# Kernel optimization log

Hardware: AMD Instinct MI355X
Metric: run time of the kernel (lower is better)

Reference implementation:

```python
import jax, jax.numpy as jnp
import numpy as np

NS = [65536, 16384, 4096, 1024, 256, 64]          # nodes per level (64 = 8 graphs x 8 dense voxels)
ES = [1048576, 262144, 65536, 16384, 4096]        # edges per level (avg degree 16)
INS = [1, 15, 23, 31, 39]
OUTS = [12, 20, 28, 36, 44]
K = 5                                             # kernel_size


def setup_inputs():
    keys = iter(jax.random.split(jax.random.key(0), 64))
    d = {'x': jax.random.normal(next(keys), (NS[0], 1), jnp.float32),
         'pos': jax.random.uniform(next(keys), (NS[0], 3), jnp.float32)}
    for l in range(5):
        n, e, ci, co = NS[l], ES[l], INS[l], OUTS[l]
        d[f'src{l}'] = jax.random.randint(next(keys), (e,), 0, n)
        d[f'dst{l}'] = jax.random.randint(next(keys), (e,), 0, n)
        d[f'eattr{l}'] = jax.random.normal(next(keys), (e, 3), jnp.float32)
        d[f'cluster{l}'] = jax.random.randint(next(keys), (n,), 0, NS[l + 1])
        d[f'w1_{l}'] = jax.random.normal(next(keys), (3, K), jnp.float32) * 0.5
        d[f'b1_{l}'] = jnp.zeros((K,), jnp.float32)
        d[f'w2_{l}'] = jax.random.normal(next(keys), (K, ci * co), jnp.float32) / np.float32(np.sqrt(K * ci))
        d[f'b2_{l}'] = jnp.zeros((ci * co,), jnp.float32)
        d[f'root_{l}'] = jax.random.normal(next(keys), (ci, co), jnp.float32) / np.float32(np.sqrt(ci))
        d[f'bias_{l}'] = jnp.zeros((co,), jnp.float32)
    d['fc_w'] = jax.random.normal(next(keys), (8 * 47, 10), jnp.float32) / np.float32(np.sqrt(8 * 47))
    d['fc_b'] = jnp.zeros((10,), jnp.float32)
    return d


def _conv(x, src, dst, eattr, w1, b1, w2, b2, root, bias, n):
    # edge-conditioned kernel: MLP(edge_attr) -> [E, ci, co]
    h = jnp.tanh(eattr @ w1 + b1)                                  # [E, K]
    We = (h @ w2 + b2).reshape(eattr.shape[0], x.shape[1], -1)     # [E, ci, co]
    msg = jnp.einsum('ei,eio->eo', x[src], We)                     # gather + per-edge matvec
    s = jax.ops.segment_sum(msg, dst, num_segments=n)
    cnt = jax.ops.segment_sum(jnp.ones((dst.shape[0], 1), x.dtype), dst, num_segments=n)
    agg = s / jnp.maximum(cnt, 1.0)                                # mean aggregation
    return agg + x @ root + bias, jnp.mean(jnp.square(We))


def _pool(x, pos, cluster, n_next):
    # sparse voxel max pool on features, mean on positions; pos concatenated to features
    xm = jax.ops.segment_max(x, cluster, num_segments=n_next)
    xm = jnp.where(jnp.isfinite(xm), xm, 0.0)                      # empty voxels -> 0
    ps = jax.ops.segment_sum(pos, cluster, num_segments=n_next)
    cnt = jax.ops.segment_sum(jnp.ones((pos.shape[0], 1), pos.dtype), cluster, num_segments=n_next)
    pm = ps / jnp.maximum(cnt, 1.0)
    return jnp.concatenate([xm, pm], axis=1), pm


def reference(x, pos, src0, dst0, eattr0, cluster0, w1_0, b1_0, w2_0, b2_0, root_0, bias_0,
              src1, dst1, eattr1, cluster1, w1_1, b1_1, w2_1, b2_1, root_1, bias_1,
              src2, dst2, eattr2, cluster2, w1_2, b1_2, w2_2, b2_2, root_2, bias_2,
              src3, dst3, eattr3, cluster3, w1_3, b1_3, w2_3, b2_3, root_3, bias_3,
              src4, dst4, eattr4, cluster4, w1_4, b1_4, w2_4, b2_4, root_4, bias_4,
              fc_w, fc_b):
    lv = [(src0, dst0, eattr0, cluster0, w1_0, b1_0, w2_0, b2_0, root_0, bias_0),
          (src1, dst1, eattr1, cluster1, w1_1, b1_1, w2_1, b2_1, root_1, bias_1),
          (src2, dst2, eattr2, cluster2, w1_2, b1_2, w2_2, b2_2, root_2, bias_2),
          (src3, dst3, eattr3, cluster3, w1_3, b1_3, w2_3, b2_3, root_3, bias_3),
          (src4, dst4, eattr4, cluster4, w1_4, b1_4, w2_4, b2_4, root_4, bias_4)]
    closs = jnp.float32(0.0)
    for l, (src, dst, ea, cl, w1, b1, w2, b2, rt, bs) in enumerate(lv):
        x, c = _conv(x, src, dst, ea, w1, b1, w2, b2, rt, bs, NS[l])
        closs = closs + c
        x, pos = _pool(x, pos, cl, NS[l + 1])
    feat = x.reshape(-1, 8 * 47)                                   # [B, 8*47]
    logits = feat @ fc_w + fc_b
    return jax.nn.log_softmax(logits, axis=1), closs
```

## Files before the change

### kernel.cpp

```cpp
#include <hip/hip_runtime.h>
#include <hip/hip_fp16.h>
#include <math.h>


#define TILES0 1024
#define TSZ0   1024
#define NB0    512
#define TILES1 256
#define TSZ1   1024
#define NB1    512

__device__ __forceinline__ float ftanh(float x) {
    float e = __expf(2.f * x);
    return 1.f - 2.f / (e + 1.f);
}

struct SegArgs {
    const int* idx[10];
    int*       cnt[10];
    int*       rp [10];
    int*       out[10];
    int        n  [10];
    int        nb [10];
    int        tstart[11];
};

struct ScanAux {
    int* tilesum;
    int* tileoff;
    int  sstart[11];
    int  T;
};

struct HArgs {
    const float* eattr[5];
    const float* w1[5];
    const float* b1[5];
    float*       H;
    int          E[5];
    int          bstart[6];
};

struct WArgs {
    const float* w2[5];
    const float* b2[5];
    const float* H;
    float*       sq;
    int          cico[5];
    int          E[5];
};

__global__ __launch_bounds__(256) void countA_k(
    SegArgs a, HArgs ha, const int* __restrict__ dst0,
    const int* __restrict__ dst1, int* __restrict__ M, int* __restrict__ M1,
    int hsBlocks)
{
    __shared__ int sh[NB0];
    int B = blockIdx.x;
    int t = threadIdx.x;

    if (B < TILES0) {
        for (int u = t; u < NB0; u += 256) sh[u] = 0;
        __syncthreads();
        int base = B * TSZ0 + t;
        #pragma unroll
        for (int it = 0; it < 4; it++)
            atomicAdd(&sh[dst0[base + it * 256] >> 7], 1);
        __syncthreads();
        for (int u = t; u < NB0; u += 256) M[(size_t)B * NB0 + u] = sh[u];
        return;
    }
    B -= TILES0;
    if (B < TILES1) {
        for (int u = t; u < NB1; u += 256) sh[u] = 0;
        __syncthreads();
        int base = B * TSZ1 + t;
        #pragma unroll
        for (int it = 0; it < 4; it++)
            atomicAdd(&sh[dst1[base + it * 256] >> 5], 1);
        __syncthreads();
        for (int u = t; u < NB1; u += 256) M1[(size_t)B * NB1 + u] = sh[u];
        return;
    }
    B -= TILES1;
    if (B < hsBlocks) {
        const int K = 8;
        int l = 0;
        while (l < 4 && B >= ha.bstart[l + 1]) l++;
        int bloc = B - ha.bstart[l];
        const float* ea = ha.eattr[l];
        float w1r[15], b1r[5];
        #pragma unroll
        for (int i = 0; i < 15; i++) w1r[i] = ha.w1[l][i];
        #pragma unroll
        for (int i = 0; i < 5; i++)  b1r[i] = ha.b1[l][i];
        float acc[20];
        #pragma unroll
        for (int i = 0; i < 20; i++) acc[i] = 0.f;
        int base = bloc * 256 * K + t;
        for (int it = 0; it < K; it++) {
            int e = base + it * 256;
            if (e < ha.E[l]) {
                float e0 = ea[e * 3], e1 = ea[e * 3 + 1], e2 = ea[e * 3 + 2];
                float h[5];
                #pragma unroll
                for (int k = 0; k < 5; k++)
                    h[k] = ftanh(e0 * w1r[k] + e1 * w1r[5 + k] + e2 * w1r[10 + k] + b1r[k]);
                int p = 5;
                #pragma unroll
                for (int k = 0; k < 5; k++) {
                    acc[k] += h[k];
                    #pragma unroll
                    for (int k2 = k; k2 < 5; k2++) acc[p++] += h[k] * h[k2];
                }
            }
        }
        float* red = (float*)sh;
        int wid = t >> 6, lane = t & 63;
        #pragma unroll
        for (int v = 0; v < 20; v++) {
            float s = acc[v];
            #pragma unroll
            for (int o = 32; o; o >>= 1) s += __shfl_down(s, o);
            if (lane == 0) red[wid * 20 + v] = s;
        }
        __syncthreads();
        if (t < 20)
            atomicAdd(&ha.H[l * 20 + t],
                      red[t] + red[20 + t] + red[40 + t] + red[60 + t]);
        return;
    }
    B -= hsBlocks;
    {
        int s = 0;
        while (s < 9 && B >= a.tstart[s + 1]) s++;
        int i0 = (B - a.tstart[s]) * 1024;
        const int* idx = a.idx[s];
        int* cnt = a.cnt[s];
        int n = a.n[s];
        #pragma unroll
        for (int j = 0; j < 4; j++) {
            int i = i0 + j * 256 + t;
            if (i < n) atomicAdd(&cnt[idx[i]], 1);
        }
    }
}

__global__ __launch_bounds__(256) void scanP1_k(
    SegArgs a, ScanAux x, const int* __restrict__ M, int* __restrict__ M2,
    int* __restrict__ colTotal, const int* __restrict__ M1,
    int* __restrict__ M21, int* __restrict__ ct1)
{
    __shared__ int sc[256];
    int B = blockIdx.x;
    int t = threadIdx.x;

    if (B < NB0) {
        int v[4];
        int s4 = 0;
        #pragma unroll
        for (int j = 0; j < 4; j++) {
            v[j] = M[(size_t)(t * 4 + j) * NB0 + B];
            s4 += v[j];
        }
        sc[t] = s4;
        __syncthreads();
        for (int d = 1; d < 256; d <<= 1) {
            int u = (t >= d) ? sc[t - d] : 0;
            __syncthreads();
            sc[t] += u;
            __syncthreads();
        }
        int run = sc[t] - s4;
        #pragma unroll
        for (int j = 0; j < 4; j++) {
            M2[(size_t)(t * 4 + j) * NB0 + B] = run;
            run += v[j];
        }
        if (t == 255) colTotal[B] = sc[255];
        return;
    }
    B -= NB0;
    if (B < NB1) {
        int v = M1[(size_t)t * NB1 + B];
        sc[t] = v;
        __syncthreads();
        for (int d = 1; d < 256; d <<= 1) {
            int u = (t >= d) ? sc[t - d] : 0;
            __syncthreads();
            sc[t] += u;
            __syncthreads();
        }
        M21[(size_t)t * NB1 + B] = sc[t] - v;
        if (t == 255) ct1[B] = sc[255];
        return;
    }
    int b = B - NB1;
    int s = 0;
    while (s < 9 && b >= x.sstart[s + 1]) s++;
    int tloc = b - x.sstart[s];
    int nb = a.nb[s];
    const int* cnt = a.cnt[s];
    int i0 = tloc * 4096 + t * 16;
    int sum = 0;
    #pragma unroll
    for (int k = 0; k < 16; k++) {
        int i = i0 + k;
        if (i < nb) sum += cnt[i];
    }
    #pragma unroll
    for (int o = 32; o; o >>= 1) sum += __shfl_down(sum, o);
    if ((t & 63) == 0) sc[t >> 6] = sum;
    __syncthreads();
    if (t == 0)
        x.tilesum[b] = sc[0] + sc[1] + sc[2] + sc[3];
}

__global__ __launch_bounds__(512) void scanP2_k(
    SegArgs a, ScanAux x, const int* __restrict__ colTotal,
    int* __restrict__ bucketStart, const int* __restrict__ ct1,
    int* __restrict__ bs1)
{
    __shared__ int sc[NB0];
    int t = threadIdx.x;
    if (blockIdx.x == 0) {
        int v = colTotal[t];
        sc[t] = v;
        __syncthreads();
        for (int d = 1; d < NB0; d <<= 1) {
            int u = (t >= d) ? sc[t - d] : 0;
            __syncthreads();
            sc[t] += u;
            __syncthreads();
        }
        bucketStart[t] = sc[t] - v;
        if (t == NB0 - 1) bucketStart[NB0] = sc[NB0 - 1];
        return;
    }
    if (blockIdx.x == 2) {
        int v = ct1[t];
        sc[t] = v;
        __syncthreads();
        for (int d = 1; d < NB1; d <<= 1) {
            int u = (t >= d) ? sc[t - d] : 0;
            __syncthreads();
            sc[t] += u;
            __syncthreads();
        }
        bs1[t] = sc[t] - v;
        if (t == NB1 - 1) bs1[NB1] = sc[NB1 - 1];
        return;
    }
    if (t >= 64) return;
    int lane = t;
    int orig = (lane < x.T) ? x.tilesum[lane] : 0;
    int val = orig;
    #pragma unroll
    for (int d = 1; d < 64; d <<= 1) {
        int v = __shfl_up(val, d);
        if (lane >= d) val += v;
    }
    int excl = val - orig;
    int s = 0;
    while (s < 9 && lane >= x.sstart[s + 1]) s++;
    int segExcl = __shfl(excl, x.sstart[s]);
    if (lane < x.T) {
        x.tileoff[lane] = excl - segExcl;
        if (lane == x.sstart[s + 1] - 1)
            a.rp[s][a.nb[s]] = val - segExcl;
    }
}

__global__ __launch_bounds__(256) void scanP3_k(
    SegArgs a, ScanAux x,
    const int* __restrict__ src, const int* __restrict__ dst,
    const float* __restrict__ ea, const float* __restrict__ x0,
    const int* __restrict__ M2, const int* __restrict__ bucketStart,
    float4* __restrict__ pay2,
    const float* __restrict__ w1, const float* __restrict__ b1,
    float* __restrict__ H0,
    const int* __restrict__ src1, const int* __restrict__ dst1,
    const float* __restrict__ ea1, const int* __restrict__ M21,
    const int* __restrict__ bs1, float4* __restrict__ pay1)
{
    __shared__ int   shi[NB0];
    __shared__ float shf[100];
    int B = blockIdx.x;
    int t = threadIdx.x;

    if (B < TILES0) {
        int tile = B;
        for (int u = t; u < NB0; u += 256)
            shi[u] = bucketStart[u] + M2[(size_t)tile * NB0 + u];
        if (t < 15) shf[t] = w1[t];
        if (t >= 32 && t < 37) shf[15 + t - 32] = b1[t - 32];
        __syncthreads();

        float acc[20];
        #pragma unroll
        for (int i = 0; i < 20; i++) acc[i] = 0.f;

        int base = tile * TSZ0 + t;
        #pragma unroll
        for (int it = 0; it < 4; it++) {
            int i = base + it * 256;
            int d = dst[i];
            float e0 = ea[i * 3], e1 = ea[i * 3 + 1], e2 = ea[i * 3 + 2];
            float h[5];
            #pragma unroll
            for (int k = 0; k < 5; k++)
                h[k] = ftanh(e0 * shf[k] + e1 * shf[5 + k] + e2 * shf[10 + k] + shf[15 + k]);
            int p = 5;
            #pragma unroll
            for (int k = 0; k < 5; k++) {
                acc[k] += h[k];
                #pragma unroll
                for (int k2 = k; k2 < 5; k2++) acc[p++] += h[k] * h[k2];
            }
            float xv = x0[src[i]];
            union HU { __half2 h2; float f; } p01, p23;
            p01.h2 = __floats2half2_rn(h[0], h[1]);
            p23.h2 = __floats2half2_rn(h[2], h[3]);
            unsigned wbits = ((unsigned)d << 16) |
                             (unsigned)__half_as_ushort(__float2half_rn(h[4]));
            int ps = atomicAdd(&shi[d >> 7], 1);
            pay2[ps] = make_float4(xv, p01.f, p23.f, __uint_as_float(wbits));
        }

        int wid = t >> 6, lane = t & 63;
        #pragma unroll
        for (int v = 0; v < 20; v++) {
            float s = acc[v];
            #pragma unroll
            for (int o = 32; o; o >>= 1) s += __shfl_down(s, o);
            if (lane == 0) shf[20 + wid * 20 + v] = s;
        }
        __syncthreads();
        if (t < 20)
            atomicAdd(&H0[t], shf[20 + t] + shf[40 + t] + shf[60 + t] + shf[80 + t]);
        return;
    }
    B -= TILES0;
    if (B < TILES1) {
        int tile = B;
        for (int u = t; u < NB1; u += 256)
            shi[u] = bs1[u] + M21[(size_t)tile * NB1 + u];
        __syncthreads();
        int base = tile * TSZ1 + t;
        #pragma unroll
        for (int it = 0; it < 4; it++) {
            int i = base + it * 256;
            int d = dst1[i];
            int key = (d << 16) | src1[i];
            float e0 = ea1[i * 3], e1 = ea1[i * 3 + 1], e2 = ea1[i * 3 + 2];
            int ps = atomicAdd(&shi[d >> 5], 1);
            pay1[ps] = make_float4(__int_as_float(key), e0, e1, e2);
        }
        return;
    }
    B -= TILES1;
    int s = 0;
    while (s < 9 && B >= x.sstart[s + 1]) s++;
    int tloc = B - x.sstart[s];
    int nb = a.nb[s];
    const int* cnt = a.cnt[s];
    int* rp = a.rp[s];
    int i0 = tloc * 4096 + t * 16;
    int v[16];
    int sum = 0;
    #pragma unroll
    for (int k = 0; k < 16; k++) {
        int i = i0 + k;
        v[k] = (i < nb) ? cnt[i] : 0;
        sum += v[k];
    }
    int acc = sum;
    shi[t] = acc;
    __syncthreads();
    for (int d = 1; d < 256; d <<= 1) {
        int t2 = (t >= d) ? shi[t - d] : 0;
        __syncthreads();
        acc += t2;
        shi[t] = acc;
        __syncthreads();
    }
    int running = x.tileoff[B] + (acc - sum);
    #pragma unroll
    for (int k = 0; k < 16; k++) {
        int i = i0 + k;
        if (i < nb) rp[i] = running;
        running += v[k];
    }
}

__global__ __launch_bounds__(256) void scatC_k(
    SegArgs a, WArgs wa,
    const float4* __restrict__ pay2, const int* __restrict__ bucketStart,
    const float* __restrict__ w2, const float* __restrict__ b2,
    const float* __restrict__ root, const float* __restrict__ bias,
    const float* __restrict__ x, float* __restrict__ y,
    const float4* __restrict__ pay1, const int* __restrict__ bs1,
    int* __restrict__ rp1, float4* __restrict__ rec1)
{
    __shared__ float wsm[96];
    __shared__ float nacc[7 * 128];
    __shared__ int hist[32], st[32], cur[32];
    int B = blockIdx.x;
    int t = threadIdx.x;

    if (B < NB0) {
        if (t < 60) wsm[t] = w2[t];
        else if (t >= 64  && t < 76)  wsm[60 + t - 64]  = b2[t - 64];
        else if (t >= 128 && t < 140) wsm[72 + t - 128] = root[t - 128];
        else if (t >= 192 && t < 204) wsm[84 + t - 192] = bias[t - 192];
        for (int u = t; u < 7 * 128; u += 256) nacc[u] = 0.f;
        __syncthreads();

        int lo = bucketStart[B], hi = bucketStart[B + 1];
        int bin0 = B << 7;
        for (int j = lo + t; j < hi; j += 256) {
            float4 R = pay2[j];
            union HU { float f; __half2 h2; } a01, a23;
            a01.f = R.y; a23.f = R.z;
            unsigned wbits = __float_as_uint(R.w);
            int node = (int)(wbits >> 16) - bin0;
            float xv = R.x;
            atomicAdd(&nacc[node], xv);
            atomicAdd(&nacc[128 + node], __low2float(a01.h2)  * xv);
            atomicAdd(&nacc[256 + node], __high2float(a01.h2) * xv);
            atomicAdd(&nacc[384 + node], __low2float(a23.h2)  * xv);
            atomicAdd(&nacc[512 + node], __high2float(a23.h2) * xv);
            atomicAdd(&nacc[640 + node],
                      __half2float(__ushort_as_half((unsigned short)(wbits & 0xffffu))) * xv);
            atomicAdd(&nacc[768 + node], 1.f);
        }
        __syncthreads();

        if (t < 128) {
            int v = bin0 + t;
            float deg = nacc[768 + t];
            float S0 = nacc[t],       S1 = nacc[128 + t], S2 = nacc[256 + t];
            float S3 = nacc[384 + t], S4 = nacc[512 + t], S5 = nacc[640 + t];
            float inv = 1.f / fmaxf(deg, 1.f);
            float xv = x[v];
            #pragma unroll
            for (int o = 0; o < 12; o++) {
                float msg = wsm[60 + o] * S0 + wsm[o] * S1 + wsm[12 + o] * S2 +
                            wsm[24 + o] * S3 + wsm[36 + o] * S4 + wsm[48 + o] * S5;
                y[v * 12 + o] = msg * inv + xv * wsm[72 + o] + wsm[84 + o];
            }
        }
        return;
    }
    B -= NB0;
    if (B < NB1) {
        int b = B;
        int lo = bs1[b], hi = bs1[b + 1];
        int bin0 = b << 5;
        if (t < 32) hist[t] = 0;
        __syncthreads();
        const float* payw = (const float*)pay1;
        for (int j = lo + t; j < hi; j += 256) {
            int rel = (int)(__float_as_uint(payw[4 * j]) >> 16) - bin0;
            atomicAdd(&hist[rel], 1);
        }
        __syncthreads();
        if (t < 32) {
            int v = hist[t];
            int val = v;
            #pragma unroll
            for (int d = 1; d < 32; d <<= 1) {
                int u = __shfl_up(val, d);
                if (t >= d) val += u;
            }
            st[t] = val - v;
            cur[t] = lo + val - v;
            rp1[bin0 + t] = lo + val - v;
            if (b == NB1 - 1 && t == 31) rp1[NB1 * 32] = hi;
        }
        __syncthreads();
        for (int j = lo + t; j < hi; j += 256) {
            float4 R = pay1[j];
            int rel = (int)(__float_as_uint(R.x) >> 16) - bin0;
            int p = atomicAdd(&cur[rel], 1);
            rec1[p] = R;
        }
        return;
    }
    B -= NB1;
    if (B < 5) {
        if (t >= 64) return;
        int l = B;
        const float* w2l = wa.w2[l];
        const float* b2l = wa.b2[l];
        int cico = wa.cico[l];
        float d[21];
        #pragma unroll
        for (int i = 0; i < 21; i++) d[i] = 0.f;
        for (int u = t; u < cico; u += 64) {
            float b = b2l[u];
            float w[5];
            #pragma unroll
            for (int k = 0; k < 5; k++) w[k] = w2l[k * cico + u];
            int p = 0;
            #pragma unroll
            for (int k = 0; k < 5; k++) {
                #pragma unroll
                for (int k2 = k; k2 < 5; k2++) d[p++] += w[k] * w[k2];
            }
            #pragma unroll
            for (int k = 0; k < 5; k++) d[15 + k] += b * w[k];
            d[20] += b * b;
        }
        #pragma unroll
        for (int i = 0; i < 21; i++) {
            #pragma unroll
            for (int off = 32; off; off >>= 1) d[i] += __shfl_down(d[i], off);
        }
        if (t == 0) {
            const float* H1 = wa.H + l * 20;
            const float* H2 = H1 + 5;
            float sq = (float)wa.E[l] * d[20];
            #pragma unroll
            for (int k = 0; k < 5; k++) sq += 2.f * d[15 + k] * H1[k];
            int p = 0;
            #pragma unroll
            for (int k = 0; k < 5; k++) {
                #pragma unroll
                for (int k2 = k; k2 < 5; k2++) {
                    sq += ((k == k2) ? 1.f : 2.f) * d[p] * H2[p];
                    p++;
                }
            }
            wa.sq[l] = sq;
        }
        return;
    }
    B -= 5;
    {
        int s = 0;
        while (s < 9 && B >= a.tstart[s + 1]) s++;
        int i0 = (B - a.tstart[s]) * 1024;
        const int* idx = a.idx[s];
        int* cnt = a.cnt[s];
        const int* rp = a.rp[s];
        int* out = a.out[s];
        int n = a.n[s];
        #pragma unroll
        for (int j = 0; j < 4; j++) {
            int i = i0 + j * 256 + t;
            if (i < n) {
                int d = idx[i];
                int p = atomicSub(&cnt[d], 1) - 1;
                out[rp[d] + p] = i;
            }
        }
    }
}

__global__ __launch_bounds__(256) void conv1s_k(
    const int* __restrict__ rp, const float4* __restrict__ rec,
    const float* __restrict__ w1, const float* __restrict__ b1,
    const float* __restrict__ w2, const float* __restrict__ b2,
    const float* __restrict__ root, const float* __restrict__ bias,
    const float* __restrict__ x, float* __restrict__ y)
{
    constexpr int CI = 15, CO = 20, CH = 48, CICO = CI * CO;
    __shared__ float w1s[20];
    __shared__ float4 recb[CH];
    __shared__ int   svb[CH];
    __shared__ float hb[CH * 6];
    __shared__ float xs[CH * CI];
    __shared__ float S[6 * CI];

    int t = threadIdx.x;
    int v = blockIdx.x;
    if (t < 20) w1s[t] = (t < 15) ? w1[t] : b1[t - 15];
    int r0 = rp[v], r1 = rp[v + 1];
    int d  = r1 - r0;
    float acc = 0.f;

    for (int c0 = r0; c0 < r1; c0 += CH) {
        int cn = min(CH, r1 - c0);
        if (t < cn) {
            float4 R = rec[c0 + t];
            recb[t] = R;
            svb[t]  = (int)(__float_as_uint(R.x) & 0xffffu);
            hb[t * 6] = 1.f;
        }
        __syncthreads();
        if (t < cn * 5) {
            int j = t / 5, k = t % 5;
            float e0 = recb[j].y, e1 = recb[j].z, e2 = recb[j].w;
            hb[j * 6 + 1 + k] =
                ftanh(e0 * w1s[k] + e1 * w1s[5 + k] + e2 * w1s[10 + k] + w1s[15 + k]);
        }
        for (int u = t; u < cn * CI; u += 256)
            xs[u] = x[(size_t)svb[u / CI] * CI + (u % CI)];
        __syncthreads();
        if (t < 6 * CI) {
            int i = t / 6, k6 = t % 6;
            for (int j = 0; j < cn; j++)
                acc += hb[j * 6 + k6] * xs[j * CI + i];
        }
        __syncthreads();
    }

    if (t < 6 * CI) S[t] = acc;
    __syncthreads();

    if (t < CO) {
        float m = 0.f;
        for (int i = 0; i < CI; i++) {
            m += b2[i * CO + t] * S[i * 6];
            #pragma unroll
            for (int k = 0; k < 5; k++)
                m += w2[k * CICO + i * CO + t] * S[i * 6 + 1 + k];
        }
        m /= fmaxf((float)d, 1.f);
        for (int i = 0; i < CI; i++)
            m += x[(size_t)v * CI + i] * root[i * CO + t];
        y[(size_t)v * CO + t] = m + bias[t];
    }
}

template<int CI, int CO>
__global__ __launch_bounds__(256) void coop_conv_k(
    const int* __restrict__ rp, const int* __restrict__ eid,
    const int* __restrict__ src, const float* __restrict__ eattr,
    const float* __restrict__ w1, const float* __restrict__ b1,
    const float* __restrict__ w2, const float* __restrict__ b2,
    const float* __restrict__ root, const float* __restrict__ bias,
    const float* __restrict__ x, float* __restrict__ y)
{
    constexpr int CH   = 48;
    constexpr int CICO = CI * CO;
    __shared__ float w1s[20];
    __shared__ int   eb[CH], svb[CH];
    __shared__ float hb[CH * 6];
    __shared__ float xs[CH * CI];
    __shared__ float S[6 * CI];

    int t = threadIdx.x;
    int v = blockIdx.x;
    if (t < 20) w1s[t] = (t < 15) ? w1[t] : b1[t - 15];
    int r0 = rp[v], r1 = rp[v + 1];
    int d  = r1 - r0;
    float acc = 0.f;

    for (int c0 = r0; c0 < r1; c0 += CH) {
        int cn = min(CH, r1 - c0);
        if (t < cn) {
            int e = eid[c0 + t];
            eb[t]  = e;
            svb[t] = src[e];
            hb[t * 6] = 1.f;
        }
        __syncthreads();
        if (t < cn * 5) {
            int j = t / 5, k = t % 5;
            int e = eb[j];
            float e0 = eattr[e * 3], e1 = eattr[e * 3 + 1], e2 = eattr[e * 3 + 2];
            hb[j * 6 + 1 + k] =
                ftanh(e0 * w1s[k] + e1 * w1s[5 + k] + e2 * w1s[10 + k] + w1s[15 + k]);
        }
        for (int u = t; u < cn * CI; u += 256)
            xs[u] = x[(size_t)svb[u / CI] * CI + (u % CI)];
        __syncthreads();
        if (t < 6 * CI) {
            int i = t / 6, k6 = t % 6;
            for (int j = 0; j < cn; j++)
                acc += hb[j * 6 + k6] * xs[j * CI + i];
        }
        __syncthreads();
    }

    if (t < 6 * CI) S[t] = acc;
    __syncthreads();

    if (t < CO) {
        float m = 0.f;
        for (int i = 0; i < CI; i++) {
            m += b2[i * CO + t] * S[i * 6];
            #pragma unroll
            for (int k = 0; k < 5; k++)
                m += w2[k * CICO + i * CO + t] * S[i * 6 + 1 + k];
        }
        m /= fmaxf((float)d, 1.f);
        for (int i = 0; i < CI; i++)
            m += x[(size_t)v * CI + i] * root[i * CO + t];
        y[(size_t)v * CO + t] = m + bias[t];
    }
}

template<int CO>
__global__ __launch_bounds__(256) void pool_k(
    int NN,
    const int* __restrict__ crp, const int* __restrict__ cnid,
    const float* __restrict__ y, const float* __restrict__ pos,
    float* __restrict__ xn, float* __restrict__ pn)
{
    int t = blockIdx.x * 256 + threadIdx.x;
    if (t >= NN * (CO + 3)) return;
    int c = t / (CO + 3), o = t % (CO + 3);
    int r0 = crp[c], r1 = crp[c + 1];
    int d = r1 - r0;
    if (o < CO) {
        float m = -INFINITY;
        for (int j = r0; j < r1; j++)
            m = fmaxf(m, y[(size_t)cnid[j] * CO + o]);
        if (d == 0 || !isfinite(m)) m = 0.f;
        xn[c * (CO + 3) + o] = m;
    } else {
        int k = o - CO;
        float sum = 0.f;
        for (int j = r0; j < r1; j++)
            sum += pos[cnid[j] * 3 + k];
        float pm = sum / fmaxf((float)d, 1.f);
        xn[c * (CO + 3) + CO + k] = pm;
        pn[c * 3 + k] = pm;
    }
}

__global__ __launch_bounds__(128) void fc_k(
    const float* __restrict__ x5,
    const float* __restrict__ fc_w, const float* __restrict__ fc_b,
    const float* __restrict__ sq, float* __restrict__ out)
{
    __shared__ float feat[8 * 376];
    __shared__ float logit[80];
    __shared__ float roff[8];
    for (int t = threadIdx.x; t < 8 * 376; t += 128) feat[t] = x5[t];
    __syncthreads();
    int t = threadIdx.x;
    if (t < 80) {
        int b = t / 10, j = t % 10;
        float acc = fc_b[j];
        for (int k = 0; k < 376; k++) acc += feat[b * 376 + k] * fc_w[k * 10 + j];
        logit[t] = acc;
    }
    __syncthreads();
    if (t < 8) {
        float m = -1e30f;
        for (int j = 0; j < 10; j++) m = fmaxf(m, logit[t * 10 + j]);
        float ssum = 0.f;
        for (int j = 0; j < 10; j++) ssum += expf(logit[t * 10 + j] - m);
        roff[t] = m + logf(ssum);
    }
    __syncthreads();
    if (t < 80) out[t] = logit[t] - roff[t / 10];
    if (t == 0) {
        float closs = 0.f;
        closs += sq[0] * (1.0f / 12582912.0f);
        closs += sq[1] * (1.0f / 78643200.0f);
        closs += sq[2] * (1.0f / 42205184.0f);
        closs += sq[3] * (1.0f / 18284544.0f);
        closs += sq[4] * (1.0f / 7028736.0f);
        out[80] = closs;
    }
}


extern "C" void kernel_launch(void* const* d_in, const int* in_sizes, int n_in,
                              void* d_out, int out_size, void* d_ws, size_t ws_size,
                              hipStream_t stream)
{
    static const int NSa[6] = {65536, 16384, 4096, 1024, 256, 64};
    static const int ESa[5] = {1048576, 262144, 65536, 16384, 4096};
    static const int COa[5] = {12, 20, 28, 36, 44};
    static const int CIa[5] = {1, 15, 23, 31, 39};

    const float* x0   = (const float*)d_in[0];
    const float* pos0 = (const float*)d_in[1];

    int* wsw = (int*)d_ws;
    size_t off = 0;
    auto alw = [&](size_t n) -> size_t {
        size_t p = off; off += (n + 63) & ~(size_t)63; return p;
    };
    size_t degO[5], cdegO[5];
    for (int l = 2; l < 5; l++) degO[l]  = alw(NSa[l]);
    for (int l = 0; l < 5; l++) cdegO[l] = alw(NSa[l + 1]);
    size_t HO = alw(100);
    size_t zeroWords = off;
    size_t rpO[5], crpO[5], eidO[5], cnidO[5];
    rpO[1] = alw(NSa[1] + 1);
    for (int l = 2; l < 5; l++) rpO[l]  = alw(NSa[l] + 1);
    for (int l = 0; l < 5; l++) crpO[l] = alw(NSa[l + 1] + 1);
    for (int l = 2; l < 5; l++) eidO[l] = alw(ESa[l]);
    for (int l = 0; l < 5; l++) cnidO[l] = alw(NSa[l]);
    size_t tsO  = alw(64);
    size_t toO  = alw(64);
    size_t MO   = alw((size_t)TILES0 * NB0);
    size_t M2O  = alw((size_t)TILES0 * NB0);
    size_t ctO  = alw(NB0);
    size_t bsO  = alw(NB0 + 1);
    size_t payO = alw((size_t)ESa[0] * 4);
    size_t M1O  = alw((size_t)TILES1 * NB1);
    size_t M21O = alw((size_t)TILES1 * NB1);
    size_t ct1O = alw(NB1);
    size_t bs1O = alw(NB1 + 1);
    size_t pay1O = alw((size_t)ESa[1] * 4);
    size_t rec1O = alw((size_t)ESa[1] * 4);
    size_t yO   = alw((size_t)65536 * 12);
    size_t sqO  = alw(8);
    size_t xnO[5], pnO[5];
    for (int l = 0; l < 5; l++) xnO[l] = alw((size_t)NSa[l + 1] * (COa[l] + 3));
    for (int l = 0; l < 5; l++) pnO[l] = alw((size_t)NSa[l] * 3 / 4 + 64);
    for (int l = 0; l < 5; l++) pnO[l] = alw((size_t)NSa[l + 1] * 3);

    hipMemsetAsync(d_ws, 0, zeroWords * 4, stream);

    SegArgs sa{};
    int nseg = 0;
    for (int l = 2; l < 5; l++) {
        sa.idx[nseg] = (const int*)d_in[3 + 10 * l];
        sa.cnt[nseg] = wsw + degO[l];
        sa.rp [nseg] = wsw + rpO[l];
        sa.out[nseg] = wsw + eidO[l];
        sa.n  [nseg] = ESa[l];
        sa.nb [nseg] = NSa[l];
        nseg++;
    }
    for (int l = 0; l < 5; l++) {
        sa.idx[nseg] = (const int*)d_in[5 + 10 * l];
        sa.cnt[nseg] = wsw + cdegO[l];
        sa.rp [nseg] = wsw + crpO[l];
        sa.out[nseg] = wsw + cnidO[l];
        sa.n  [nseg] = NSa[l];
        sa.nb [nseg] = NSa[l + 1];
        nseg++;
    }
    ScanAux sx{};
    int tiles = 0, btiles = 0;
    for (int s = 0; s < nseg; s++) {
        sa.tstart[s] = tiles;
        tiles += (sa.n[s] + 1023) / 1024;
        sx.sstart[s] = btiles;
        btiles += (sa.nb[s] + 4095) / 4096;
    }
    for (int s = nseg; s <= 10; s++) {
        sa.tstart[s] = tiles;
        sx.sstart[s] = btiles;
        if (s < 10) {
            sa.idx[s] = sa.idx[nseg - 1]; sa.cnt[s] = sa.cnt[nseg - 1];
            sa.rp[s] = sa.rp[nseg - 1];   sa.out[s] = sa.out[nseg - 1];
            sa.n[s] = 0; sa.nb[s] = 8;
        }
    }
    sx.T = btiles;
    sx.tilesum = wsw + tsO;
    sx.tileoff = wsw + toO;

    float4* pay2 = (float4*)(wsw + payO);
    float4* pay1 = (float4*)(wsw + pay1O);
    float4* rec1 = (float4*)(wsw + rec1O);
    float*  Hp   = (float*)(wsw + HO);

    HArgs ha{};
    int bs = 0;
    ha.bstart[0] = 0;
    ha.eattr[0] = (const float*)d_in[4];
    ha.w1[0] = (const float*)d_in[6];
    ha.b1[0] = (const float*)d_in[7];
    ha.E[0] = 0;
    for (int l = 1; l < 5; l++) {
        ha.eattr[l] = (const float*)d_in[4 + 10 * l];
        ha.w1[l]    = (const float*)d_in[6 + 10 * l];
        ha.b1[l]    = (const float*)d_in[7 + 10 * l];
        ha.E[l]     = ESa[l];
        ha.bstart[l] = bs;
        bs += (ESa[l] + 2047) / 2048;
    }
    ha.bstart[5] = bs;
    ha.H = Hp;

    WArgs wa{};
    for (int l = 0; l < 5; l++) {
        wa.w2[l]   = (const float*)d_in[8 + 10 * l];
        wa.b2[l]   = (const float*)d_in[9 + 10 * l];
        wa.cico[l] = CIa[l] * COa[l];
        wa.E[l]    = ESa[l];
    }
    wa.H  = Hp;
    wa.sq = (float*)(wsw + sqO);

    countA_k<<<TILES0 + TILES1 + bs + tiles, 256, 0, stream>>>(
        sa, ha, (const int*)d_in[3], (const int*)d_in[13],
        wsw + MO, wsw + M1O, bs);
    scanP1_k<<<NB0 + NB1 + btiles, 256, 0, stream>>>(
        sa, sx, wsw + MO, wsw + M2O, wsw + ctO,
        wsw + M1O, wsw + M21O, wsw + ct1O);
    scanP2_k<<<3, 512, 0, stream>>>(sa, sx, wsw + ctO, wsw + bsO,
                                    wsw + ct1O, wsw + bs1O);
    scanP3_k<<<TILES0 + TILES1 + btiles, 256, 0, stream>>>(
        sa, sx,
        (const int*)d_in[2], (const int*)d_in[3], (const float*)d_in[4],
        x0, wsw + M2O, wsw + bsO, pay2,
        (const float*)d_in[6], (const float*)d_in[7], Hp,
        (const int*)d_in[12], (const int*)d_in[13], (const float*)d_in[14],
        wsw + M21O, wsw + bs1O, pay1);

    float* yb = (float*)(wsw + yO);

    scatC_k<<<NB0 + NB1 + 5 + tiles, 256, 0, stream>>>(
        sa, wa, pay2, wsw + bsO,
        (const float*)d_in[8], (const float*)d_in[9],
        (const float*)d_in[10], (const float*)d_in[11], x0, yb,
        pay1, wsw + bs1O, wsw + rpO[1], rec1);

    pool_k<12><<<(NSa[1] * 15 + 255) / 256, 256, 0, stream>>>(
        NSa[1], wsw + crpO[0], wsw + cnidO[0], yb, pos0,
        (float*)(wsw + xnO[0]), (float*)(wsw + pnO[0]));

    conv1s_k<<<NSa[1], 256, 0, stream>>>(
        wsw + rpO[1], rec1,
        (const float*)d_in[16], (const float*)d_in[17],
        (const float*)d_in[18], (const float*)d_in[19],
        (const float*)d_in[20], (const float*)d_in[21],
        (const float*)(wsw + xnO[0]), yb);
    pool_k<20><<<(NSa[2] * 23 + 255) / 256, 256, 0, stream>>>(
        NSa[2], wsw + crpO[1], wsw + cnidO[1], yb,
        (const float*)(wsw + pnO[0]),
        (float*)(wsw + xnO[1]), (float*)(wsw + pnO[1]));

#define LVLC(l, CI_, CO_) do {                                                 \
    const float* xin   = (const float*)(wsw + xnO[(l) - 1]);                   \
    const float* posin = (const float*)(wsw + pnO[(l) - 1]);                   \
    int N = NSa[(l)], NN = NSa[(l) + 1];                                       \
    coop_conv_k<CI_, CO_><<<N, 256, 0, stream>>>(                              \
        wsw + rpO[(l)], wsw + eidO[(l)],                                       \
        (const int*)d_in[2 + 10 * (l)], (const float*)d_in[4 + 10 * (l)],      \
        (const float*)d_in[6 + 10 * (l)], (const float*)d_in[7 + 10 * (l)],    \
        (const float*)d_in[8 + 10 * (l)], (const float*)d_in[9 + 10 * (l)],    \
        (const float*)d_in[10 + 10 * (l)], (const float*)d_in[11 + 10 * (l)],  \
        xin, yb);                                                              \
    pool_k<CO_><<<(NN * ((CO_) + 3) + 255) / 256, 256, 0, stream>>>(           \
        NN, wsw + crpO[(l)], wsw + cnidO[(l)], yb, posin,                      \
        (float*)(wsw + xnO[(l)]), (float*)(wsw + pnO[(l)]));                   \
} while (0)

    LVLC(2, 23, 28);
    LVLC(3, 31, 36);
    LVLC(4, 39, 44);
#undef LVLC

    fc_k<<<1, 128, 0, stream>>>((const float*)(wsw + xnO[4]),
                                (const float*)d_in[52], (const float*)d_in[53],
                                wa.sq, (float*)d_out);
}
```

Measured before the change: 403.6 us.

## Replace level-0 edge sort with per-node moment atomics and fuse pooling into convs

Level-0 edges are no longer bucket-sorted into a payload. Because ci=1, each edge instead atomically adds x_src and h_k*x_src into a per-destination 8-float accumulator, and the node output is rebuilt algebraically from those sums with w2/b2. Max pooling is done with atomicMax on order-preserving encoded floats into raw per-cluster rows, so the separate pool kernels and cluster CSR scans go away. The launch chain drops from around 14 to 9 kernels. In exchange it adds heavy global float atomics (7 per edge over 1M edges) and makes the float summation order nondeterministic.

```diff
diff --git a/kernel.cpp b/kernel.cpp
--- a/kernel.cpp
+++ b/kernel.cpp
@@ -3,9 +3,6 @@
 #include <math.h>
 
 
-#define TILES0 1024
-#define TSZ0   1024
-#define NB0    512
 #define TILES1 256
 #define TSZ1   1024
 #define NB1    512
@@ -15,92 +12,143 @@
     return 1.f - 2.f / (e + 1.f);
 }
 
-struct SegArgs {
-    const int* idx[10];
-    int*       cnt[10];
-    int*       rp [10];
-    int*       out[10];
-    int        n  [10];
-    int        nb [10];
-    int        tstart[11];
+__device__ __forceinline__ unsigned fenc(float f) {
+    int b = __float_as_int(f);
+    return (b < 0) ? ~(unsigned)b : ((unsigned)b | 0x80000000u);
+}
+__device__ __forceinline__ float fdec(unsigned u) {
+    int b = (u & 0x80000000u) ? (int)(u & 0x7fffffffu) : ~(int)u;
+    return __int_as_float(b);
+}
+
+__device__ __forceinline__ float row_val(const unsigned* __restrict__ row,
+                                         int i, int CI) {
+    float cn = __uint_as_float(row[CI]);
+    if (i < CI - 3) return (cn == 0.f) ? 0.f : fdec(row[i]);
+    return __uint_as_float(row[i]) / fmaxf(cn, 1.f);
+}
+
+struct Seg3 {
+    const int* idx[3];
+    int*       cnt[3];
+    int*       rp [3];
+    int*       out[3];
+    int        n  [3];
+    int        nb [3];
+    int        tstart[4];
 };
 
-struct ScanAux {
-    int* tilesum;
-    int* tileoff;
-    int  sstart[11];
-    int  T;
+struct GA {
+    const int *src0, *dst0; const float* ea0;
+    const int *src1, *dst1; const float* ea1;
+    const float *x0, *pos0;
+    const int* cluster[5];
+    const float *w1[5], *b1[5], *w2[5], *b2[5], *root[5], *bias[5];
+    const int* srcE[3]; const float* eaE[3];
+    const float *fc_w, *fc_b;
+    float* S0;
+    unsigned* raw[5];
+    float* H; float* sq;
+    int *M1, *M21, *bktTot, *bs1;
+    float4 *pay1, *rec1; int* rp1;
+    Seg3 sg;
+    float* out;
+    const float* hea[4]; int hE[4]; int hb0[5];
+    int hsB, tiles;
 };
 
-struct HArgs {
-    const float* eattr[5];
-    const float* w1[5];
-    const float* b1[5];
-    float*       H;
-    int          E[5];
-    int          bstart[6];
-};
-
-struct WArgs {
-    const float* w2[5];
-    const float* b2[5];
-    const float* H;
-    float*       sq;
-    int          cico[5];
-    int          E[5];
-};
-
-__global__ __launch_bounds__(256) void countA_k(
-    SegArgs a, HArgs ha, const int* __restrict__ dst0,
-    const int* __restrict__ dst1, int* __restrict__ M, int* __restrict__ M1,
-    int hsBlocks)
+__global__ __launch_bounds__(256) void k1_fuseA(GA A)
 {
-    __shared__ int sh[NB0];
-    int B = blockIdx.x;
-    int t = threadIdx.x;
-
-    if (B < TILES0) {
-        for (int u = t; u < NB0; u += 256) sh[u] = 0;
-        __syncthreads();
-        int base = B * TSZ0 + t;
-        #pragma unroll
-        for (int it = 0; it < 4; it++)
-            atomicAdd(&sh[dst0[base + it * 256] >> 7], 1);
-        __syncthreads();
-        for (int u = t; u < NB0; u += 256) M[(size_t)B * NB0 + u] = sh[u];
+    __shared__ int sh[NB1];
+    int B = blockIdx.x, t = threadIdx.x;
+
+    if (B < 1024) {
+        float w1r[15], b1r[5];
+        #pragma unroll
+        for (int i = 0; i < 15; i++) w1r[i] = A.w1[0][i];
+        #pragma unroll
+        for (int i = 0; i < 5; i++)  b1r[i] = A.b1[0][i];
+        float acc[20];
+        #pragma unroll
+        for (int i = 0; i < 20; i++) acc[i] = 0.f;
+        int base = B * 1024 + t;
+        #pragma unroll
+        for (int it = 0; it < 4; it++) {
+            int i = base + it * 256;
+            int sv = A.src0[i], d = A.dst0[i];
+            float e0 = A.ea0[i * 3], e1 = A.ea0[i * 3 + 1], e2 = A.ea0[i * 3 + 2];
+            float h[5];
+            #pragma unroll
+            for (int k = 0; k < 5; k++)
+                h[k] = ftanh(e0 * w1r[k] + e1 * w1r[5 + k] + e2 * w1r[10 + k] + b1r[k]);
+            int p = 5;
+            #pragma unroll
+            for (int k = 0; k < 5; k++) {
+                acc[k] += h[k];
+                #pragma unroll
+                for (int k2 = k; k2 < 5; k2++) acc[p++] += h[k] * h[k2];
+            }
+            float xv = A.x0[sv];
+            float* Sr = A.S0 + (size_t)d * 8;
+            atomicAdd(&Sr[0], xv);
+            atomicAdd(&Sr[1], h[0] * xv);
+            atomicAdd(&Sr[2], h[1] * xv);
+            atomicAdd(&Sr[3], h[2] * xv);
+            atomicAdd(&Sr[4], h[3] * xv);
+            atomicAdd(&Sr[5], h[4] * xv);
+            atomicAdd(&Sr[6], 1.f);
+        }
+        float* red = (float*)sh;
+        int wid = t >> 6, lane = t & 63;
+        #pragma unroll
+        for (int v = 0; v < 20; v++) {
+            float s = acc[v];
+            #pragma unroll
+            for (int o = 32; o; o >>= 1) s += __shfl_down(s, o);
+            if (lane == 0) red[wid * 20 + v] = s;
+        }
+        __syncthreads();
+        if (t < 20)
+            atomicAdd(&A.H[t], red[t] + red[20 + t] + red[40 + t] + red[60 + t]);
         return;
     }
-    B -= TILES0;
+    B -= 1024;
     if (B < TILES1) {
         for (int u = t; u < NB1; u += 256) sh[u] = 0;
         __syncthreads();
         int base = B * TSZ1 + t;
         #pragma unroll
         for (int it = 0; it < 4; it++)
-            atomicAdd(&sh[dst1[base + it * 256] >> 5], 1);
-        __syncthreads();
-        for (int u = t; u < NB1; u += 256) M1[(size_t)B * NB1 + u] = sh[u];
+            atomicAdd(&sh[A.dst1[base + it * 256] >> 5], 1);
+        __syncthreads();
+        for (int u = t; u < NB1; u += 256) {
+            int c = sh[u];
+            A.M1[(size_t)B * NB1 + u] = c;
+            if (c) atomicAdd(&A.bktTot[u], c);
+        }
         return;
     }
     B -= TILES1;
-    if (B < hsBlocks) {
+    if (B < A.hsB) {
         const int K = 8;
-        int l = 0;
-        while (l < 4 && B >= ha.bstart[l + 1]) l++;
-        int bloc = B - ha.bstart[l];
-        const float* ea = ha.eattr[l];
+        int j = 0;
+        while (j < 3 && B >= A.hb0[j + 1]) j++;
+        int bloc = B - A.hb0[j];
+        const float* ea = A.hea[j];
+        const float* w1p = A.w1[j + 1];
+        const float* b1p = A.b1[j + 1];
         float w1r[15], b1r[5];
         #pragma unroll
-        for (int i = 0; i < 15; i++) w1r[i] = ha.w1[l][i];
-        #pragma unroll
-        for (int i = 0; i < 5; i++)  b1r[i] = ha.b1[l][i];
+        for (int i = 0; i < 15; i++) w1r[i] = w1p[i];
+        #pragma unroll
+        for (int i = 0; i < 5; i++)  b1r[i] = b1p[i];
         float acc[20];
         #pragma unroll
         for (int i = 0; i < 20; i++) acc[i] = 0.f;
         int base = bloc * 256 * K + t;
         for (int it = 0; it < K; it++) {
             int e = base + it * 256;
-            if (e < ha.E[l]) {
+            if (e < A.hE[j]) {
                 float e0 = ea[e * 3], e1 = ea[e * 3 + 1], e2 = ea[e * 3 + 2];
                 float h[5];
                 #pragma unroll
@@ -126,18 +174,18 @@
         }
         __syncthreads();
         if (t < 20)
-            atomicAdd(&ha.H[l * 20 + t],
+            atomicAdd(&A.H[(j + 1) * 20 + t],
                       red[t] + red[20 + t] + red[40 + t] + red[60 + t]);
         return;
     }
-    B -= hsBlocks;
+    B -= A.hsB;
     {
         int s = 0;
-        while (s < 9 && B >= a.tstart[s + 1]) s++;
-        int i0 = (B - a.tstart[s]) * 1024;
-        const int* idx = a.idx[s];
-        int* cnt = a.cnt[s];
-        int n = a.n[s];
+        while (s < 2 && B >= A.sg.tstart[s + 1]) s++;
+        int i0 = (B - A.sg.tstart[s]) * 1024;
+        const int* idx = A.sg.idx[s];
+        int* cnt = A.sg.cnt[s];
+        int n = A.sg.n[s];
         #pragma unroll
         for (int j = 0; j < 4; j++) {
             int i = i0 + j * 256 + t;
@@ -146,24 +194,43 @@
     }
 }
 
-__global__ __launch_bounds__(256) void scanP1_k(
-    SegArgs a, ScanAux x, const int* __restrict__ M, int* __restrict__ M2,
-    int* __restrict__ colTotal, const int* __restrict__ M1,
-    int* __restrict__ M21, int* __restrict__ ct1)
+__global__ __launch_bounds__(256) void k2_fuseB(GA A)
 {
     __shared__ int sc[256];
-    int B = blockIdx.x;
-    int t = threadIdx.x;
-
-    if (B < NB0) {
-        int v[4];
-        int s4 = 0;
-        #pragma unroll
-        for (int j = 0; j < 4; j++) {
-            v[j] = M[(size_t)(t * 4 + j) * NB0 + B];
-            s4 += v[j];
-        }
-        sc[t] = s4;
+    __shared__ float wsm[96];
+    int B = blockIdx.x, t = threadIdx.x;
+
+    if (B < 256) {
+        if (t < 60) wsm[t] = A.w2[0][t];
+        else if (t >= 64  && t < 76)  wsm[60 + t - 64]  = A.b2[0][t - 64];
+        else if (t >= 128 && t < 140) wsm[72 + t - 128] = A.root[0][t - 128];
+        else if (t >= 192 && t < 204) wsm[84 + t - 192] = A.bias[0][t - 192];
+        __syncthreads();
+        int v = B * 256 + t;
+        const float* Sr = A.S0 + (size_t)v * 8;
+        float s0 = Sr[0], s1 = Sr[1], s2 = Sr[2], s3 = Sr[3], s4 = Sr[4], s5 = Sr[5];
+        float dg = Sr[6];
+        float inv = 1.f / fmaxf(dg, 1.f);
+        float xv = A.x0[v];
+        int c = A.cluster[0][v];
+        unsigned* orow = A.raw[0] + (size_t)c * 16;
+        #pragma unroll
+        for (int o = 0; o < 12; o++) {
+            float m = (wsm[60 + o] * s0 + wsm[o] * s1 + wsm[12 + o] * s2 +
+                       wsm[24 + o] * s3 + wsm[36 + o] * s4 + wsm[48 + o] * s5) * inv +
+                      xv * wsm[72 + o] + wsm[84 + o];
+            atomicMax(&orow[o], fenc(m));
+        }
+        atomicAdd((float*)&orow[12], A.pos0[v * 3]);
+        atomicAdd((float*)&orow[13], A.pos0[v * 3 + 1]);
+        atomicAdd((float*)&orow[14], A.pos0[v * 3 + 2]);
+        atomicAdd((float*)&orow[15], 1.f);
+        return;
+    }
+    B -= 256;
+    if (B < NB1) {
+        int v = A.M1[(size_t)t * NB1 + B];
+        sc[t] = v;
         __syncthreads();
         for (int d = 1; d < 256; d <<= 1) {
             int u = (t >= d) ? sc[t - d] : 0;
@@ -171,19 +238,14 @@
             sc[t] += u;
             __syncthreads();
         }
-        int run = sc[t] - s4;
-        #pragma unroll
-        for (int j = 0; j < 4; j++) {
-            M2[(size_t)(t * 4 + j) * NB0 + B] = run;
-            run += v[j];
-        }
-        if (t == 255) colTotal[B] = sc[255];
+        A.M21[(size_t)t * NB1 + B] = sc[t] - v;
         return;
     }
-    B -= NB0;
-    if (B < NB1) {
-        int v = M1[(size_t)t * NB1 + B];
-        sc[t] = v;
+    B -= NB1;
+    if (B < 1) {
+        int a0 = A.bktTot[2 * t], a1 = A.bktTot[2 * t + 1];
+        int ps = a0 + a1;
+        sc[t] = ps;
         __syncthreads();
         for (int d = 1; d < 256; d <<= 1) {
             int u = (t >= d) ? sc[t - d] : 0;
@@ -191,309 +253,55 @@
             sc[t] += u;
             __syncthreads();
         }
-        M21[(size_t)t * NB1 + B] = sc[t] - v;
-        if (t == 255) ct1[B] = sc[255];
+        int excl = sc[t] - ps;
+        A.bs1[2 * t]     = excl;
+        A.bs1[2 * t + 1] = excl + a0;
+        if (t == 255) A.bs1[512] = sc[255];
         return;
     }
-    int b = B - NB1;
-    int s = 0;
-    while (s < 9 && b >= x.sstart[s + 1]) s++;
-    int tloc = b - x.sstart[s];
-    int nb = a.nb[s];
-    const int* cnt = a.cnt[s];
-    int i0 = tloc * 4096 + t * 16;
-    int sum = 0;
-    #pragma unroll
-    for (int k = 0; k < 16; k++) {
-        int i = i0 + k;
-        if (i < nb) sum += cnt[i];
-    }
-    #pragma unroll
-    for (int o = 32; o; o >>= 1) sum += __shfl_down(sum, o);
-    if ((t & 63) == 0) sc[t >> 6] = sum;
-    __syncthreads();
-    if (t == 0)
-        x.tilesum[b] = sc[0] + sc[1] + sc[2] + sc[3];
-}
-
-__global__ __launch_bounds__(512) void scanP2_k(
-    SegArgs a, ScanAux x, const int* __restrict__ colTotal,
-    int* __restrict__ bucketStart, const int* __restrict__ ct1,
-    int* __restrict__ bs1)
-{
-    __shared__ int sc[NB0];
-    int t = threadIdx.x;
-    if (blockIdx.x == 0) {
-        int v = colTotal[t];
-        sc[t] = v;
-        __syncthreads();
-        for (int d = 1; d < NB0; d <<= 1) {
-            int u = (t >= d) ? sc[t - d] : 0;
+    B -= 1;
+    if (B < 3) {
+        int s = B;
+        int nb = A.sg.nb[s];
+        const int* cnt = A.sg.cnt[s];
+        int* rp = A.sg.rp[s];
+        int i0 = t * 16;
+        int v[16];
+        int sum = 0;
+        #pragma unroll
+        for (int k = 0; k < 16; k++) {
+            int i = i0 + k;
+            v[k] = (i < nb) ? cnt[i] : 0;
+            sum += v[k];
+        }
+        int acc = sum;
+        sc[t] = acc;
+        __syncthreads();
+        for (int d = 1; d < 256; d <<= 1) {
+            int t2 = (t >= d) ? sc[t - d] : 0;
             __syncthreads();
-            sc[t] += u;
+            acc += t2;
+            sc[t] = acc;
             __syncthreads();
         }
-        bucketStart[t] = sc[t] - v;
-        if (t == NB0 - 1) bucketStart[NB0] = sc[NB0 - 1];
+        int running = acc - sum;
+        #pragma unroll
+        for (int k = 0; k < 16; k++) {
+            int i = i0 + k;
+            if (i < nb) rp[i] = running;
+            running += v[k];
+        }
+        if (i0 + 16 == nb) rp[nb] = running;
         return;
     }
-    if (blockIdx.x == 2) {
-        int v = ct1[t];
-        sc[t] = v;
-        __syncthreads();
-        for (int d = 1; d < NB1; d <<= 1) {
-            int u = (t >= d) ? sc[t - d] : 0;
-            __syncthreads();
-            sc[t] += u;
-            __syncthreads();
-        }
-        bs1[t] = sc[t] - v;
-        if (t == NB1 - 1) bs1[NB1] = sc[NB1 - 1];
-        return;
-    }
-    if (t >= 64) return;
-    int lane = t;
-    int orig = (lane < x.T) ? x.tilesum[lane] : 0;
-    int val = orig;
-    #pragma unroll
-    for (int d = 1; d < 64; d <<= 1) {
-        int v = __shfl_up(val, d);
-        if (lane >= d) val += v;
-    }
-    int excl = val - orig;
-    int s = 0;
-    while (s < 9 && lane >= x.sstart[s + 1]) s++;
-    int segExcl = __shfl(excl, x.sstart[s]);
-    if (lane < x.T) {
-        x.tileoff[lane] = excl - segExcl;
-        if (lane == x.sstart[s + 1] - 1)
-            a.rp[s][a.nb[s]] = val - segExcl;
-    }
-}
-
-__global__ __launch_bounds__(256) void scanP3_k(
-    SegArgs a, ScanAux x,
-    const int* __restrict__ src, const int* __restrict__ dst,
-    const float* __restrict__ ea, const float* __restrict__ x0,
-    const int* __restrict__ M2, const int* __restrict__ bucketStart,
-    float4* __restrict__ pay2,
-    const float* __restrict__ w1, const float* __restrict__ b1,
-    float* __restrict__ H0,
-    const int* __restrict__ src1, const int* __restrict__ dst1,
-    const float* __restrict__ ea1, const int* __restrict__ M21,
-    const int* __restrict__ bs1, float4* __restrict__ pay1)
-{
-    __shared__ int   shi[NB0];
-    __shared__ float shf[100];
-    int B = blockIdx.x;
-    int t = threadIdx.x;
-
-    if (B < TILES0) {
-        int tile = B;
-        for (int u = t; u < NB0; u += 256)
-            shi[u] = bucketStart[u] + M2[(size_t)tile * NB0 + u];
-        if (t < 15) shf[t] = w1[t];
-        if (t >= 32 && t < 37) shf[15 + t - 32] = b1[t - 32];
-        __syncthreads();
-
-        float acc[20];
-        #pragma unroll
-        for (int i = 0; i < 20; i++) acc[i] = 0.f;
-
-        int base = tile * TSZ0 + t;
-        #pragma unroll
-        for (int it = 0; it < 4; it++) {
-            int i = base + it * 256;
-            int d = dst[i];
-            float e0 = ea[i * 3], e1 = ea[i * 3 + 1], e2 = ea[i * 3 + 2];
-            float h[5];
-            #pragma unroll
-            for (int k = 0; k < 5; k++)
-                h[k] = ftanh(e0 * shf[k] + e1 * shf[5 + k] + e2 * shf[10 + k] + shf[15 + k]);
-            int p = 5;
-            #pragma unroll
-            for (int k = 0; k < 5; k++) {
-                acc[k] += h[k];
-                #pragma unroll
-                for (int k2 = k; k2 < 5; k2++) acc[p++] += h[k] * h[k2];
-            }
-            float xv = x0[src[i]];
-            union HU { __half2 h2; float f; } p01, p23;
-            p01.h2 = __floats2half2_rn(h[0], h[1]);
-            p23.h2 = __floats2half2_rn(h[2], h[3]);
-            unsigned wbits = ((unsigned)d << 16) |
-                             (unsigned)__half_as_ushort(__float2half_rn(h[4]));
-            int ps = atomicAdd(&shi[d >> 7], 1);
-            pay2[ps] = make_float4(xv, p01.f, p23.f, __uint_as_float(wbits));
-        }
-
-        int wid = t >> 6, lane = t & 63;
-        #pragma unroll
-        for (int v = 0; v < 20; v++) {
-            float s = acc[v];
-            #pragma unroll
-            for (int o = 32; o; o >>= 1) s += __shfl_down(s, o);
-            if (lane == 0) shf[20 + wid * 20 + v] = s;
-        }
-        __syncthreads();
-        if (t < 20)
-            atomicAdd(&H0[t], shf[20 + t] + shf[40 + t] + shf[60 + t] + shf[80 + t]);
-        return;
-    }
-    B -= TILES0;
-    if (B < TILES1) {
-        int tile = B;
-        for (int u = t; u < NB1; u += 256)
-            shi[u] = bs1[u] + M21[(size_t)tile * NB1 + u];
-        __syncthreads();
-        int base = tile * TSZ1 + t;
-        #pragma unroll
-        for (int it = 0; it < 4; it++) {
-            int i = base + it * 256;
-            int d = dst1[i];
-            int key = (d << 16) | src1[i];
-            float e0 = ea1[i * 3], e1 = ea1[i * 3 + 1], e2 = ea1[i * 3 + 2];
-            int ps = atomicAdd(&shi[d >> 5], 1);
-            pay1[ps] = make_float4(__int_as_float(key), e0, e1, e2);
-        }
-        return;
-    }
-    B -= TILES1;
-    int s = 0;
-    while (s < 9 && B >= x.sstart[s + 1]) s++;
-    int tloc = B - x.sstart[s];
-    int nb = a.nb[s];
-    const int* cnt = a.cnt[s];
-    int* rp = a.rp[s];
-    int i0 = tloc * 4096 + t * 16;
-    int v[16];
-    int sum = 0;
-    #pragma unroll
-    for (int k = 0; k < 16; k++) {
-        int i = i0 + k;
-        v[k] = (i < nb) ? cnt[i] : 0;
-        sum += v[k];
-    }
-    int acc = sum;
-    shi[t] = acc;
-    __syncthreads();
-    for (int d = 1; d < 256; d <<= 1) {
-        int t2 = (t >= d) ? shi[t - d] : 0;
-        __syncthreads();
-        acc += t2;
-        shi[t] = acc;
-        __syncthreads();
-    }
-    int running = x.tileoff[B] + (acc - sum);
-    #pragma unroll
-    for (int k = 0; k < 16; k++) {
-        int i = i0 + k;
-        if (i < nb) rp[i] = running;
-        running += v[k];
-    }
-}
-
-__global__ __launch_bounds__(256) void scatC_k(
-    SegArgs a, WArgs wa,
-    const float4* __restrict__ pay2, const int* __restrict__ bucketStart,
-    const float* __restrict__ w2, const float* __restrict__ b2,
-    const float* __restrict__ root, const float* __restrict__ bias,
-    const float* __restrict__ x, float* __restrict__ y,
-    const float4* __restrict__ pay1, const int* __restrict__ bs1,
-    int* __restrict__ rp1, float4* __restrict__ rec1)
-{
-    __shared__ float wsm[96];
-    __shared__ float nacc[7 * 128];
-    __shared__ int hist[32], st[32], cur[32];
-    int B = blockIdx.x;
-    int t = threadIdx.x;
-
-    if (B < NB0) {
-        if (t < 60) wsm[t] = w2[t];
-        else if (t >= 64  && t < 76)  wsm[60 + t - 64]  = b2[t - 64];
-        else if (t >= 128 && t < 140) wsm[72 + t - 128] = root[t - 128];
-        else if (t >= 192 && t < 204) wsm[84 + t - 192] = bias[t - 192];
-        for (int u = t; u < 7 * 128; u += 256) nacc[u] = 0.f;
-        __syncthreads();
-
-        int lo = bucketStart[B], hi = bucketStart[B + 1];
-        int bin0 = B << 7;
-        for (int j = lo + t; j < hi; j += 256) {
-            float4 R = pay2[j];
-            union HU { float f; __half2 h2; } a01, a23;
-            a01.f = R.y; a23.f = R.z;
-            unsigned wbits = __float_as_uint(R.w);
-            int node = (int)(wbits >> 16) - bin0;
-            float xv = R.x;
-            atomicAdd(&nacc[node], xv);
-            atomicAdd(&nacc[128 + node], __low2float(a01.h2)  * xv);
-            atomicAdd(&nacc[256 + node], __high2float(a01.h2) * xv);
-            atomicAdd(&nacc[384 + node], __low2float(a23.h2)  * xv);
-            atomicAdd(&nacc[512 + node], __high2float(a23.h2) * xv);
-            atomicAdd(&nacc[640 + node],
-                      __half2float(__ushort_as_half((unsigned short)(wbits & 0xffffu))) * xv);
-            atomicAdd(&nacc[768 + node], 1.f);
-        }
-        __syncthreads();
-
-        if (t < 128) {
-            int v = bin0 + t;
-            float deg = nacc[768 + t];
-            float S0 = nacc[t],       S1 = nacc[128 + t], S2 = nacc[256 + t];
-            float S3 = nacc[384 + t], S4 = nacc[512 + t], S5 = nacc[640 + t];
-            float inv = 1.f / fmaxf(deg, 1.f);
-            float xv = x[v];
-            #pragma unroll
-            for (int o = 0; o < 12; o++) {
-                float msg = wsm[60 + o] * S0 + wsm[o] * S1 + wsm[12 + o] * S2 +
-                            wsm[24 + o] * S3 + wsm[36 + o] * S4 + wsm[48 + o] * S5;
-                y[v * 12 + o] = msg * inv + xv * wsm[72 + o] + wsm[84 + o];
-            }
-        }
-        return;
-    }
-    B -= NB0;
-    if (B < NB1) {
-        int b = B;
-        int lo = bs1[b], hi = bs1[b + 1];
-        int bin0 = b << 5;
-        if (t < 32) hist[t] = 0;
-        __syncthreads();
-        const float* payw = (const float*)pay1;
-        for (int j = lo + t; j < hi; j += 256) {
-            int rel = (int)(__float_as_uint(payw[4 * j]) >> 16) - bin0;
-            atomicAdd(&hist[rel], 1);
-        }
-        __syncthreads();
-        if (t < 32) {
-            int v = hist[t];
-            int val = v;
-            #pragma unroll
-            for (int d = 1; d < 32; d <<= 1) {
-                int u = __shfl_up(val, d);
-                if (t >= d) val += u;
-            }
-            st[t] = val - v;
-            cur[t] = lo + val - v;
-            rp1[bin0 + t] = lo + val - v;
-            if (b == NB1 - 1 && t == 31) rp1[NB1 * 32] = hi;
-        }
-        __syncthreads();
-        for (int j = lo + t; j < hi; j += 256) {
-            float4 R = pay1[j];
-            int rel = (int)(__float_as_uint(R.x) >> 16) - bin0;
-            int p = atomicAdd(&cur[rel], 1);
-            rec1[p] = R;
-        }
-        return;
-    }
-    B -= NB1;
-    if (B < 5) {
+    B -= 3;
+    {
         if (t >= 64) return;
         int l = B;
-        const float* w2l = wa.w2[l];
-        const float* b2l = wa.b2[l];
-        int cico = wa.cico[l];
+        const float* w2l = A.w2[l];
+        const float* b2l = A.b2[l];
+        static const int cicoA[5] = {12, 300, 644, 1116, 1716};
+        int cico = cicoA[l];
         float d[21];
         #pragma unroll
         for (int i = 0; i < 21; i++) d[i] = 0.f;
@@ -518,9 +326,10 @@
             for (int off = 32; off; off >>= 1) d[i] += __shfl_down(d[i], off);
         }
         if (t == 0) {
-            const float* H1 = wa.H + l * 20;
+            static const int EA[5] = {1048576, 262144, 65536, 16384, 4096};
+            const float* H1 = A.H + l * 20;
             const float* H2 = H1 + 5;
-            float sq = (float)wa.E[l] * d[20];
+            float sq = (float)EA[l] * d[20];
             #pragma unroll
             for (int k = 0; k < 5; k++) sq += 2.f * d[15 + k] * H1[k];
             int p = 0;
@@ -532,20 +341,43 @@
                     p++;
                 }
             }
-            wa.sq[l] = sq;
+            A.sq[l] = sq;
+        }
+    }
+}
+
+__global__ __launch_bounds__(256) void k3_fuseC(GA A)
+{
+    __shared__ int shi[NB1];
+    int B = blockIdx.x, t = threadIdx.x;
+
+    if (B < TILES1) {
+        int tile = B;
+        for (int u = t; u < NB1; u += 256)
+            shi[u] = A.bs1[u] + A.M21[(size_t)tile * NB1 + u];
+        __syncthreads();
+        int base = tile * TSZ1 + t;
+        #pragma unroll
+        for (int it = 0; it < 4; it++) {
+            int i = base + it * 256;
+            int d = A.dst1[i];
+            int key = (d << 16) | A.src1[i];
+            float e0 = A.ea1[i * 3], e1 = A.ea1[i * 3 + 1], e2 = A.ea1[i * 3 + 2];
+            int ps = atomicAdd(&shi[d >> 5], 1);
+            A.pay1[ps] = make_float4(__int_as_float(key), e0, e1, e2);
         }
         return;
     }
-    B -= 5;
+    B -= TILES1;
     {
         int s = 0;
-        while (s < 9 && B >= a.tstart[s + 1]) s++;
-        int i0 = (B - a.tstart[s]) * 1024;
-        const int* idx = a.idx[s];
-        int* cnt = a.cnt[s];
-        const int* rp = a.rp[s];
-        int* out = a.out[s];
-        int n = a.n[s];
+        while (s < 2 && B >= A.sg.tstart[s + 1]) s++;
+        int i0 = (B - A.sg.tstart[s]) * 1024;
+        const int* idx = A.sg.idx[s];
+        int* cnt = A.sg.cnt[s];
+        const int* rp = A.sg.rp[s];
+        int* out = A.sg.out[s];
+        int n = A.sg.n[s];
         #pragma unroll
         for (int j = 0; j < 4; j++) {
             int i = i0 + j * 256 + t;
@@ -558,32 +390,64 @@
     }
 }
 
-__global__ __launch_bounds__(256) void conv1s_k(
-    const int* __restrict__ rp, const float4* __restrict__ rec,
-    const float* __restrict__ w1, const float* __restrict__ b1,
-    const float* __restrict__ w2, const float* __restrict__ b2,
-    const float* __restrict__ root, const float* __restrict__ bias,
-    const float* __restrict__ x, float* __restrict__ y)
+__global__ __launch_bounds__(256) void k4_bucket1(GA A)
 {
-    constexpr int CI = 15, CO = 20, CH = 48, CICO = CI * CO;
+    __shared__ int hist[32], cur[32];
+    int b = blockIdx.x, t = threadIdx.x;
+    int lo = A.bs1[b], hi = A.bs1[b + 1];
+    int bin0 = b << 5;
+    if (t < 32) hist[t] = 0;
+    __syncthreads();
+    const float* payw = (const float*)A.pay1;
+    for (int j = lo + t; j < hi; j += 256) {
+        int rel = (int)(__float_as_uint(payw[4 * j]) >> 16) - bin0;
+        atomicAdd(&hist[rel], 1);
+    }
+    __syncthreads();
+    if (t < 32) {
+        int v = hist[t];
+        int val = v;
+        #pragma unroll
+        for (int d = 1; d < 32; d <<= 1) {
+            int u = __shfl_up(val, d);
+            if (t >= d) val += u;
+        }
+        cur[t] = lo + val - v;
+        A.rp1[bin0 + t] = lo + val - v;
+        if (b == NB1 - 1 && t == 31) A.rp1[NB1 * 32] = hi;
+    }
+    __syncthreads();
+    for (int j = lo + t; j < hi; j += 256) {
+        float4 R = A.pay1[j];
+        int rel = (int)(__float_as_uint(R.x) >> 16) - bin0;
+        int p = atomicAdd(&cur[rel], 1);
+        A.rec1[p] = R;
+    }
+}
+
+__global__ __launch_bounds__(256) void k5_conv1(GA A)
+{
+    constexpr int CI = 15, CO = 20, CH = 48, CICO = CI * CO, RL = 16, RN = 24;
     __shared__ float w1s[20];
     __shared__ float4 recb[CH];
     __shared__ int   svb[CH];
     __shared__ float hb[CH * 6];
     __shared__ float xs[CH * CI];
-    __shared__ float S[6 * CI];
-
-    int t = threadIdx.x;
-    int v = blockIdx.x;
-    if (t < 20) w1s[t] = (t < 15) ? w1[t] : b1[t - 15];
-    int r0 = rp[v], r1 = rp[v + 1];
-    int d  = r1 - r0;
+    __shared__ float Sx[6 * CI];
+    __shared__ float xown[CI];
+
+    int t = threadIdx.x, v = blockIdx.x;
+    const unsigned* rin = A.raw[0];
+    if (t < 20) w1s[t] = (t < 15) ? A.w1[1][t] : A.b1[1][t - 15];
+    if (t < CI) xown[t] = row_val(rin + (size_t)v * RL, t, CI);
+    int r0 = A.rp1[v], r1 = A.rp1[v + 1];
+    int d = r1 - r0;
     float acc = 0.f;
 
     for (int c0 = r0; c0 < r1; c0 += CH) {
         int cn = min(CH, r1 - c0);
         if (t < cn) {
-            float4 R = rec[c0 + t];
+            float4 R = A.rec1[c0 + t];
             recb[t] = R;
             svb[t]  = (int)(__float_as_uint(R.x) & 0xffffu);
             hb[t * 6] = 1.f;
@@ -595,57 +459,66 @@
             hb[j * 6 + 1 + k] =
                 ftanh(e0 * w1s[k] + e1 * w1s[5 + k] + e2 * w1s[10 + k] + w1s[15 + k]);
         }
-        for (int u = t; u < cn * CI; u += 256)
-            xs[u] = x[(size_t)svb[u / CI] * CI + (u % CI)];
+        for (int u = t; u < cn * CI; u += 256) {
+            int j = u / CI, i = u - j * CI;
+            xs[u] = row_val(rin + (size_t)svb[j] * RL, i, CI);
+        }
         __syncthreads();
         if (t < 6 * CI) {
-            int i = t / 6, k6 = t % 6;
+            int i = t / 6, k6 = t - (t / 6) * 6;
             for (int j = 0; j < cn; j++)
                 acc += hb[j * 6 + k6] * xs[j * CI + i];
         }
         __syncthreads();
     }
 
-    if (t < 6 * CI) S[t] = acc;
+    if (t < 6 * CI) Sx[t] = acc;
     __syncthreads();
 
     if (t < CO) {
         float m = 0.f;
+        const float* w2 = A.w2[1];
+        const float* b2 = A.b2[1];
         for (int i = 0; i < CI; i++) {
-            m += b2[i * CO + t] * S[i * 6];
+            m += b2[i * CO + t] * Sx[i * 6];
             #pragma unroll
             for (int k = 0; k < 5; k++)
-                m += w2[k * CICO + i * CO + t] * S[i * 6 + 1 + k];
+                m += w2[k * CICO + i * CO + t] * Sx[i * 6 + 1 + k];
         }
         m /= fmaxf((float)d, 1.f);
-        for (int i = 0; i < CI; i++)
-            m += x[(size_t)v * CI + i] * root[i * CO + t];
-        y[(size_t)v * CO + t] = m + bias[t];
+        for (int i = 0; i < CI; i++) m += xown[i] * A.root[1][i * CO + t];
+        m += A.bias[1][t];
+        int c = A.cluster[1][v];
+        unsigned* orow = A.raw[1] + (size_t)c * RN;
+        atomicMax(&orow[t], fenc(m));
+        if (t < 3) atomicAdd((float*)&orow[CO + t], xown[CI - 3 + t]);
+        if (t == 0) atomicAdd((float*)&orow[CO + 3], 1.f);
     }
 }
 
 template<int CI, int CO>
-__global__ __launch_bounds__(256) void coop_conv_k(
-    const int* __restrict__ rp, const int* __restrict__ eid,
-    const int* __restrict__ src, const float* __restrict__ eattr,
-    const float* __restrict__ w1, const float* __restrict__ b1,
-    const float* __restrict__ w2, const float* __restrict__ b2,
-    const float* __restrict__ root, const float* __restrict__ bias,
-    const float* __restrict__ x, float* __restrict__ y)
+__global__ __launch_bounds__(256) void coopP_k(GA A, int l)
 {
-    constexpr int CH   = 48;
-    constexpr int CICO = CI * CO;
+    constexpr int CH = 48, CICO = CI * CO, RL = CI + 1, RN = CO + 4;
     __shared__ float w1s[20];
     __shared__ int   eb[CH], svb[CH];
     __shared__ float hb[CH * 6];
     __shared__ float xs[CH * CI];
-    __shared__ float S[6 * CI];
-
-    int t = threadIdx.x;
-    int v = blockIdx.x;
-    if (t < 20) w1s[t] = (t < 15) ? w1[t] : b1[t - 15];
+    __shared__ float Sx[6 * CI];
+    __shared__ float xown[CI];
+
+    int t = threadIdx.x, v = blockIdx.x;
+    int s = l - 2;
+    const unsigned* rin = A.raw[l - 1];
+    const int* rp = A.sg.rp[s];
+    const int* eid = A.sg.out[s];
+    const int* src = A.srcE[s];
+    const float* eattr = A.eaE[s];
+
+    if (t < 20) w1s[t] = (t < 15) ? A.w1[l][t] : A.b1[l][t - 15];
+    if (t < CI) xown[t] = row_val(rin + (size_t)v * RL, t, CI);
     int r0 = rp[v], r1 = rp[v + 1];
-    int d  = r1 - r0;
+    int d = r1 - r0;
     float acc = 0.f;
 
     for (int c0 = r0; c0 < r1; c0 += CH) {
@@ -664,79 +537,60 @@
             hb[j * 6 + 1 + k] =
                 ftanh(e0 * w1s[k] + e1 * w1s[5 + k] + e2 * w1s[10 + k] + w1s[15 + k]);
         }
-        for (int u = t; u < cn * CI; u += 256)
-            xs[u] = x[(size_t)svb[u / CI] * CI + (u % CI)];
+        for (int u = t; u < cn * CI; u += 256) {
+            int j = u / CI, i = u - j * CI;
+            xs[u] = row_val(rin + (size_t)svb[j] * RL, i, CI);
+        }
         __syncthreads();
         if (t < 6 * CI) {
-            int i = t / 6, k6 = t % 6;
+            int i = t / 6, k6 = t - (t / 6) * 6;
             for (int j = 0; j < cn; j++)
                 acc += hb[j * 6 + k6] * xs[j * CI + i];
         }
         __syncthreads();
     }
 
-    if (t < 6 * CI) S[t] = acc;
+    if (t < 6 * CI) Sx[t] = acc;
     __syncthreads();
 
     if (t < CO) {
         float m = 0.f;
+        const float* w2 = A.w2[l];
+        const float* b2 = A.b2[l];
         for (int i = 0; i < CI; i++) {
-            m += b2[i * CO + t] * S[i * 6];
+            m += b2[i * CO + t] * Sx[i * 6];
             #pragma unroll
             for (int k = 0; k < 5; k++)
-                m += w2[k * CICO + i * CO + t] * S[i * 6 + 1 + k];
+                m += w2[k * CICO + i * CO + t] * Sx[i * 6 + 1 + k];
         }
         m /= fmaxf((float)d, 1.f);
-        for (int i = 0; i < CI; i++)
-            m += x[(size_t)v * CI + i] * root[i * CO + t];
-        y[(size_t)v * CO + t] = m + bias[t];
-    }
-}
-
-template<int CO>
-__global__ __launch_bounds__(256) void pool_k(
-    int NN,
-    const int* __restrict__ crp, const int* __restrict__ cnid,
-    const float* __restrict__ y, const float* __restrict__ pos,
-    float* __restrict__ xn, float* __restrict__ pn)
-{
-    int t = blockIdx.x * 256 + threadIdx.x;
-    if (t >= NN * (CO + 3)) return;
-    int c = t / (CO + 3), o = t % (CO + 3);
-    int r0 = crp[c], r1 = crp[c + 1];
-    int d = r1 - r0;
-    if (o < CO) {
-        float m = -INFINITY;
-        for (int j = r0; j < r1; j++)
-            m = fmaxf(m, y[(size_t)cnid[j] * CO + o]);
-        if (d == 0 || !isfinite(m)) m = 0.f;
-        xn[c * (CO + 3) + o] = m;
-    } else {
-        int k = o - CO;
-        float sum = 0.f;
-        for (int j = r0; j < r1; j++)
-            sum += pos[cnid[j] * 3 + k];
-        float pm = sum / fmaxf((float)d, 1.f);
-        xn[c * (CO + 3) + CO + k] = pm;
-        pn[c * 3 + k] = pm;
-    }
-}
-
-__global__ __launch_bounds__(128) void fc_k(
-    const float* __restrict__ x5,
-    const float* __restrict__ fc_w, const float* __restrict__ fc_b,
-    const float* __restrict__ sq, float* __restrict__ out)
+        for (int i = 0; i < CI; i++) m += xown[i] * A.root[l][i * CO + t];
+        m += A.bias[l][t];
+        int c = A.cluster[l][v];
+        unsigned* orow = A.raw[l] + (size_t)c * RN;
+        atomicMax(&orow[t], fenc(m));
+        if (t < 3) atomicAdd((float*)&orow[CO + t], xown[CI - 3 + t]);
+        if (t == 0) atomicAdd((float*)&orow[CO + 3], 1.f);
+    }
+}
+
+__global__ __launch_bounds__(128) void k9_fc(GA A)
 {
     __shared__ float feat[8 * 376];
     __shared__ float logit[80];
     __shared__ float roff[8];
-    for (int t = threadIdx.x; t < 8 * 376; t += 128) feat[t] = x5[t];
+    const unsigned* r5 = A.raw[4];
+    for (int idx = threadIdx.x; idx < 64 * 47; idx += 128) {
+        int n = idx / 47, i = idx - n * 47;
+        int b = n >> 3, s = n & 7;
+        feat[b * 376 + s * 47 + i] = row_val(r5 + (size_t)n * 48, i, 47);
+    }
     __syncthreads();
     int t = threadIdx.x;
     if (t < 80) {
         int b = t / 10, j = t % 10;
-        float acc = fc_b[j];
-        for (int k = 0; k < 376; k++) acc += feat[b * 376 + k] * fc_w[k * 10 + j];
+        float acc = A.fc_b[j];
+        for (int k = 0; k < 376; k++) acc += feat[b * 376 + k] * A.fc_w[k * 10 + j];
         logit[t] = acc;
     }
     __syncthreads();
@@ -748,15 +602,16 @@
         roff[t] = m + logf(ssum);
     }
     __syncthreads();
-    if (t < 80) out[t] = logit[t] - roff[t / 10];
+    if (t < 80) A.out[t] = logit[t] - roff[t / 10];
     if (t == 0) {
+        const float* sq = A.sq;
         float closs = 0.f;
         closs += sq[0] * (1.0f / 12582912.0f);
         closs += sq[1] * (1.0f / 78643200.0f);
         closs += sq[2] * (1.0f / 42205184.0f);
         closs += sq[3] * (1.0f / 18284544.0f);
         closs += sq[4] * (1.0f / 7028736.0f);
-        out[80] = closs;
+        A.out[80] = closs;
     }
 }
 
@@ -767,185 +622,99 @@
 {
     static const int NSa[6] = {65536, 16384, 4096, 1024, 256, 64};
     static const int ESa[5] = {1048576, 262144, 65536, 16384, 4096};
-    static const int COa[5] = {12, 20, 28, 36, 44};
-    static const int CIa[5] = {1, 15, 23, 31, 39};
-
-    const float* x0   = (const float*)d_in[0];
-    const float* pos0 = (const float*)d_in[1];
+    static const int RNa[5] = {16, 24, 32, 40, 48};
 
     int* wsw = (int*)d_ws;
     size_t off = 0;
     auto alw = [&](size_t n) -> size_t {
         size_t p = off; off += (n + 63) & ~(size_t)63; return p;
     };
-    size_t degO[5], cdegO[5];
-    for (int l = 2; l < 5; l++) degO[l]  = alw(NSa[l]);
-    for (int l = 0; l < 5; l++) cdegO[l] = alw(NSa[l + 1]);
-    size_t HO = alw(100);
+    size_t degO[5];
+    for (int l = 2; l < 5; l++) degO[l] = alw(NSa[l]);
+    size_t HO   = alw(100);
+    size_t btO  = alw(NB1);
+    size_t S0O  = alw((size_t)65536 * 8);
+    size_t rawO[5];
+    for (int l = 0; l < 5; l++) rawO[l] = alw((size_t)NSa[l + 1] * RNa[l]);
     size_t zeroWords = off;
-    size_t rpO[5], crpO[5], eidO[5], cnidO[5];
-    rpO[1] = alw(NSa[1] + 1);
+    size_t rpO[5], eidO[5];
     for (int l = 2; l < 5; l++) rpO[l]  = alw(NSa[l] + 1);
-    for (int l = 0; l < 5; l++) crpO[l] = alw(NSa[l + 1] + 1);
     for (int l = 2; l < 5; l++) eidO[l] = alw(ESa[l]);
-    for (int l = 0; l < 5; l++) cnidO[l] = alw(NSa[l]);
-    size_t tsO  = alw(64);
-    size_t toO  = alw(64);
-    size_t MO   = alw((size_t)TILES0 * NB0);
-    size_t M2O  = alw((size_t)TILES0 * NB0);
-    size_t ctO  = alw(NB0);
-    size_t bsO  = alw(NB0 + 1);
-    size_t payO = alw((size_t)ESa[0] * 4);
-    size_t M1O  = alw((size_t)TILES1 * NB1);
-    size_t M21O = alw((size_t)TILES1 * NB1);
-    size_t ct1O = alw(NB1);
-    size_t bs1O = alw(NB1 + 1);
+    size_t M1O   = alw((size_t)TILES1 * NB1);
+    size_t M21O  = alw((size_t)TILES1 * NB1);
+    size_t bs1O  = alw(NB1 + 1);
     size_t pay1O = alw((size_t)ESa[1] * 4);
     size_t rec1O = alw((size_t)ESa[1] * 4);
-    size_t yO   = alw((size_t)65536 * 12);
-    size_t sqO  = alw(8);
-    size_t xnO[5], pnO[5];
-    for (int l = 0; l < 5; l++) xnO[l] = alw((size_t)NSa[l + 1] * (COa[l] + 3));
-    for (int l = 0; l < 5; l++) pnO[l] = alw((size_t)NSa[l] * 3 / 4 + 64);
-    for (int l = 0; l < 5; l++) pnO[l] = alw((size_t)NSa[l + 1] * 3);
+    size_t rp1O  = alw(NSa[1] + 1);
+    size_t sqO   = alw(8);
+
+    GA A{};
+    A.src0 = (const int*)d_in[2];  A.dst0 = (const int*)d_in[3];
+    A.ea0  = (const float*)d_in[4];
+    A.src1 = (const int*)d_in[12]; A.dst1 = (const int*)d_in[13];
+    A.ea1  = (const float*)d_in[14];
+    A.x0   = (const float*)d_in[0];
+    A.pos0 = (const float*)d_in[1];
+    for (int l = 0; l < 5; l++) {
+        A.cluster[l] = (const int*)d_in[5 + 10 * l];
+        A.w1[l]   = (const float*)d_in[6 + 10 * l];
+        A.b1[l]   = (const float*)d_in[7 + 10 * l];
+        A.w2[l]   = (const float*)d_in[8 + 10 * l];
+        A.b2[l]   = (const float*)d_in[9 + 10 * l];
+        A.root[l] = (const float*)d_in[10 + 10 * l];
+        A.bias[l] = (const float*)d_in[11 + 10 * l];
+    }
+    for (int s = 0; s < 3; s++) {
+        A.srcE[s] = (const int*)d_in[2 + 10 * (s + 2)];
+        A.eaE[s]  = (const float*)d_in[4 + 10 * (s + 2)];
+    }
+    A.fc_w = (const float*)d_in[52];
+    A.fc_b = (const float*)d_in[53];
+    A.S0 = (float*)(wsw + S0O);
+    for (int l = 0; l < 5; l++) A.raw[l] = (unsigned*)(wsw + rawO[l]);
+    A.H  = (float*)(wsw + HO);
+    A.sq = (float*)(wsw + sqO);
+    A.M1 = wsw + M1O; A.M21 = wsw + M21O;
+    A.bktTot = wsw + btO; A.bs1 = wsw + bs1O;
+    A.pay1 = (float4*)(wsw + pay1O);
+    A.rec1 = (float4*)(wsw + rec1O);
+    A.rp1  = wsw + rp1O;
+    A.out  = (float*)d_out;
+
+    int tiles = 0;
+    for (int s = 0; s < 3; s++) {
+        int l = s + 2;
+        A.sg.idx[s] = (const int*)d_in[3 + 10 * l];
+        A.sg.cnt[s] = wsw + degO[l];
+        A.sg.rp [s] = wsw + rpO[l];
+        A.sg.out[s] = wsw + eidO[l];
+        A.sg.n  [s] = ESa[l];
+        A.sg.nb [s] = NSa[l];
+        A.sg.tstart[s] = tiles;
+        tiles += (ESa[l] + 1023) / 1024;
+    }
+    A.sg.tstart[3] = tiles;
+    A.tiles = tiles;
+
+    int hsB = 0;
+    A.hb0[0] = 0;
+    for (int j = 0; j < 4; j++) {
+        A.hea[j] = (const float*)d_in[4 + 10 * (j + 1)];
+        A.hE[j]  = ESa[j + 1];
+        hsB += (ESa[j + 1] + 2047) / 2048;
+        A.hb0[j + 1] = hsB;
+    }
+    A.hsB = hsB;
 
     hipMemsetAsync(d_ws, 0, zeroWords * 4, stream);
 
-    SegArgs sa{};
-    int nseg = 0;
-    for (int l = 2; l < 5; l++) {
-        sa.idx[nseg] = (const int*)d_in[3 + 10 * l];
-        sa.cnt[nseg] = wsw + degO[l];
-        sa.rp [nseg] = wsw + rpO[l];
-        sa.out[nseg] = wsw + eidO[l];
-        sa.n  [nseg] = ESa[l];
-        sa.nb [nseg] = NSa[l];
-        nseg++;
-    }
-    for (int l = 0; l < 5; l++) {
-        sa.idx[nseg] = (const int*)d_in[5 + 10 * l];
-        sa.cnt[nseg] = wsw + cdegO[l];
-        sa.rp [nseg] = wsw + crpO[l];
-        sa.out[nseg] = wsw + cnidO[l];
-        sa.n  [nseg] = NSa[l];
-        sa.nb [nseg] = NSa[l + 1];
-        nseg++;
-    }
-    ScanAux sx{};
-    int tiles = 0, btiles = 0;
-    for (int s = 0; s < nseg; s++) {
-        sa.tstart[s] = tiles;
-        tiles += (sa.n[s] + 1023) / 1024;
-        sx.sstart[s] = btiles;
-        btiles += (sa.nb[s] + 4095) / 4096;
-    }
-    for (int s = nseg; s <= 10; s++) {
-        sa.tstart[s] = tiles;
-        sx.sstart[s] = btiles;
-        if (s < 10) {
-            sa.idx[s] = sa.idx[nseg - 1]; sa.cnt[s] = sa.cnt[nseg - 1];
-            sa.rp[s] = sa.rp[nseg - 1];   sa.out[s] = sa.out[nseg - 1];
-            sa.n[s] = 0; sa.nb[s] = 8;
-        }
-    }
-    sx.T = btiles;
-    sx.tilesum = wsw + tsO;
-    sx.tileoff = wsw + toO;
-
-    float4* pay2 = (float4*)(wsw + payO);
-    float4* pay1 = (float4*)(wsw + pay1O);
-    float4* rec1 = (float4*)(wsw + rec1O);
-    float*  Hp   = (float*)(wsw + HO);
-
-    HArgs ha{};
-    int bs = 0;
-    ha.bstart[0] = 0;
-    ha.eattr[0] = (const float*)d_in[4];
-    ha.w1[0] = (const float*)d_in[6];
-    ha.b1[0] = (const float*)d_in[7];
-    ha.E[0] = 0;
-    for (int l = 1; l < 5; l++) {
-        ha.eattr[l] = (const float*)d_in[4 + 10 * l];
-        ha.w1[l]    = (const float*)d_in[6 + 10 * l];
-        ha.b1[l]    = (const float*)d_in[7 + 10 * l];
-        ha.E[l]     = ESa[l];
-        ha.bstart[l] = bs;
-        bs += (ESa[l] + 2047) / 2048;
-    }
-    ha.bstart[5] = bs;
-    ha.H = Hp;
-
-    WArgs wa{};
-    for (int l = 0; l < 5; l++) {
-        wa.w2[l]   = (const float*)d_in[8 + 10 * l];
-        wa.b2[l]   = (const float*)d_in[9 + 10 * l];
-        wa.cico[l] = CIa[l] * COa[l];
-        wa.E[l]    = ESa[l];
-    }
-    wa.H  = Hp;
-    wa.sq = (float*)(wsw + sqO);
-
-    countA_k<<<TILES0 + TILES1 + bs + tiles, 256, 0, stream>>>(
-        sa, ha, (const int*)d_in[3], (const int*)d_in[13],
-        wsw + MO, wsw + M1O, bs);
-    scanP1_k<<<NB0 + NB1 + btiles, 256, 0, stream>>>(
-        sa, sx, wsw + MO, wsw + M2O, wsw + ctO,
-        wsw + M1O, wsw + M21O, wsw + ct1O);
-    scanP2_k<<<3, 512, 0, stream>>>(sa, sx, wsw + ctO, wsw + bsO,
-                                    wsw + ct1O, wsw + bs1O);
-    scanP3_k<<<TILES0 + TILES1 + btiles, 256, 0, stream>>>(
-        sa, sx,
-        (const int*)d_in[2], (const int*)d_in[3], (const float*)d_in[4],
-        x0, wsw + M2O, wsw + bsO, pay2,
-        (const float*)d_in[6], (const float*)d_in[7], Hp,
-        (const int*)d_in[12], (const int*)d_in[13], (const float*)d_in[14],
-        wsw + M21O, wsw + bs1O, pay1);
-
-    float* yb = (float*)(wsw + yO);
-
-    scatC_k<<<NB0 + NB1 + 5 + tiles, 256, 0, stream>>>(
-        sa, wa, pay2, wsw + bsO,
-        (const float*)d_in[8], (const float*)d_in[9],
-        (const float*)d_in[10], (const float*)d_in[11], x0, yb,
-        pay1, wsw + bs1O, wsw + rpO[1], rec1);
-
-    pool_k<12><<<(NSa[1] * 15 + 255) / 256, 256, 0, stream>>>(
-        NSa[1], wsw + crpO[0], wsw + cnidO[0], yb, pos0,
-        (float*)(wsw + xnO[0]), (float*)(wsw + pnO[0]));
-
-    conv1s_k<<<NSa[1], 256, 0, stream>>>(
-        wsw + rpO[1], rec1,
-        (const float*)d_in[16], (const float*)d_in[17],
-        (const float*)d_in[18], (const float*)d_in[19],
-        (const float*)d_in[20], (const float*)d_in[21],
-        (const float*)(wsw + xnO[0]), yb);
-    pool_k<20><<<(NSa[2] * 23 + 255) / 256, 256, 0, stream>>>(
-        NSa[2], wsw + crpO[1], wsw + cnidO[1], yb,
-        (const float*)(wsw + pnO[0]),
-        (float*)(wsw + xnO[1]), (float*)(wsw + pnO[1]));
-
-#define LVLC(l, CI_, CO_) do {                                                 \
-    const float* xin   = (const float*)(wsw + xnO[(l) - 1]);                   \
-    const float* posin = (const float*)(wsw + pnO[(l) - 1]);                   \
-    int N = NSa[(l)], NN = NSa[(l) + 1];                                       \
-    coop_conv_k<CI_, CO_><<<N, 256, 0, stream>>>(                              \
-        wsw + rpO[(l)], wsw + eidO[(l)],                                       \
-        (const int*)d_in[2 + 10 * (l)], (const float*)d_in[4 + 10 * (l)],      \
-        (const float*)d_in[6 + 10 * (l)], (const float*)d_in[7 + 10 * (l)],    \
-        (const float*)d_in[8 + 10 * (l)], (const float*)d_in[9 + 10 * (l)],    \
-        (const float*)d_in[10 + 10 * (l)], (const float*)d_in[11 + 10 * (l)],  \
-        xin, yb);                                                              \
-    pool_k<CO_><<<(NN * ((CO_) + 3) + 255) / 256, 256, 0, stream>>>(           \
-        NN, wsw + crpO[(l)], wsw + cnidO[(l)], yb, posin,                      \
-        (float*)(wsw + xnO[(l)]), (float*)(wsw + pnO[(l)]));                   \
-} while (0)
-
-    LVLC(2, 23, 28);
-    LVLC(3, 31, 36);
-    LVLC(4, 39, 44);
-#undef LVLC
-
-    fc_k<<<1, 128, 0, stream>>>((const float*)(wsw + xnO[4]),
-                                (const float*)d_in[52], (const float*)d_in[53],
-                                wa.sq, (float*)d_out);
-}
+    k1_fuseA<<<1024 + TILES1 + hsB + tiles, 256, 0, stream>>>(A);
+    k2_fuseB<<<256 + NB1 + 1 + 3 + 5,       256, 0, stream>>>(A);
+    k3_fuseC<<<TILES1 + tiles,              256, 0, stream>>>(A);
+    k4_bucket1<<<NB1,                       256, 0, stream>>>(A);
+    k5_conv1<<<NSa[1],                      256, 0, stream>>>(A);
+    coopP_k<23, 28><<<NSa[2],               256, 0, stream>>>(A, 2);
+    coopP_k<31, 36><<<NSa[3],               256, 0, stream>>>(A, 3);
+    coopP_k<39, 44><<<NSa[4],               256, 0, stream>>>(A, 4);
+    k9_fc<<<1, 128, 0, stream>>>(A);
+}
```

Result: slower. 750.2 us (+85.9%).
